# Kernel tuning notes

Measured on AMD Instinct MI355X. Metric: run time of the kernel, lower is better.

## Reference

```python
import jax, jax.numpy as jnp
import numpy as np

B, S, D, H = 2, 2048, 2048, 16
HD = D // H          # 128
HALF = HD // 2       # 64
EPS = 1e-6


def setup_inputs() -> dict:
    key = jax.random.key(0)
    ks = jax.random.split(key, 10)
    x = jax.random.normal(ks[0], (B, S, D), jnp.float32)
    # RoPE frequencies: standard theta=10000, per (position, half head dim)
    inv_freq = 1.0 / (10000.0 ** (np.arange(HALF, dtype=np.float64) / HALF))
    ang = np.outer(np.arange(S, dtype=np.float64), inv_freq)  # (S, HALF)
    freqs_cos = jnp.asarray(np.cos(ang), jnp.float32)[:, None, :]  # (S,1,HALF)
    freqs_sin = jnp.asarray(np.sin(ang), jnp.float32)[:, None, :]
    sc = 0.02
    qw = jax.random.normal(ks[1], (D, D), jnp.float32) * sc
    kw = jax.random.normal(ks[2], (D, D), jnp.float32) * sc
    vw = jax.random.normal(ks[3], (D, D), jnp.float32) * sc
    ow = jax.random.normal(ks[4], (D, D), jnp.float32) * sc
    qb = jax.random.normal(ks[5], (D,), jnp.float32) * sc
    kb = jax.random.normal(ks[6], (D,), jnp.float32) * sc
    vb = jax.random.normal(ks[7], (D,), jnp.float32) * sc
    ob = jax.random.normal(ks[8], (D,), jnp.float32) * sc
    qnorm_w = jnp.ones((D,), jnp.float32)
    knorm_w = jnp.ones((D,), jnp.float32)
    return {"x": x, "freqs_cos": freqs_cos, "freqs_sin": freqs_sin,
            "qw": qw, "qb": qb, "kw": kw, "kb": kb, "vw": vw, "vb": vb,
            "ow": ow, "ob": ob, "qnorm_w": qnorm_w, "knorm_w": knorm_w}


def _rmsnorm(h, w):
    # norm in fp32 over full last dim (dim, not per-head), as in the source
    hf = h.astype(jnp.float32)
    inv = jax.lax.rsqrt(jnp.mean(hf * hf, axis=-1, keepdims=True) + EPS)
    return (hf * inv).astype(h.dtype) * w


def _rope(h, cos, sin):
    # h: (B,S,D) -> complex rotation on interleaved pairs per head
    b, s, _ = h.shape
    hp = h.reshape(b, s, H, HALF, 2)
    x1, x2 = hp[..., 0], hp[..., 1]
    c = cos[None]   # (1,S,1,HALF) broadcasts over batch & heads
    sn = sin[None]
    o1 = x1 * c - x2 * sn
    o2 = x1 * sn + x2 * c
    return jnp.stack([o1, o2], axis=-1).reshape(b, s, H * HD)


def reference(x, freqs_cos, freqs_sin, qw, qb, kw, kb, vw, vb, ow, ob, qnorm_w, knorm_w):
    q = _rope(_rmsnorm(x @ qw.T + qb, qnorm_w), freqs_cos, freqs_sin)
    k = _rope(_rmsnorm(x @ kw.T + kb, knorm_w), freqs_cos, freqs_sin)
    v = x @ vw.T + vb
    b, s, _ = x.shape
    qh = q.reshape(b, s, H, HD)
    kh = k.reshape(b, s, H, HD)
    vh = v.reshape(b, s, H, HD)
    scale = 1.0 / jnp.sqrt(jnp.float32(HD))
    att = jnp.einsum('bqhd,bkhd->bhqk', qh, kh) * scale
    p = jax.nn.softmax(att, axis=-1)
    o = jnp.einsum('bhqk,bkhd->bqhd', p, vh).reshape(b, s, D)
    return o @ ow.T + ob
```

## Files before the change

### kernel.cpp

```cpp
#include <hip/hip_runtime.h>
#include <stdint.h>

#define B_SZ 2
#define S_LEN 2048
#define D_DIM 2048
#define NHEAD 16
#define HD 128
#define HALF 64
#define MROWS (B_SZ * S_LEN)

typedef __attribute__((ext_vector_type(8))) __bf16 bf16x8;
typedef __attribute__((ext_vector_type(8))) unsigned short u16x8;
typedef __attribute__((ext_vector_type(4))) float f32x4;
typedef __attribute__((ext_vector_type(16))) float f32x16;
typedef __attribute__((ext_vector_type(4))) unsigned int u32x4;

__device__ inline unsigned short f2bf(float x) {
  union { float f; uint32_t u; } c; c.f = x;
  uint32_t r = (c.u + 0x7fffu + ((c.u >> 16) & 1u)) >> 16;
  return (unsigned short)r;
}

__device__ inline float bf2f(unsigned short b) {
  union { uint32_t u; float f; } c; c.u = (uint32_t)b << 16;
  return c.f;
}

__device__ inline void gll16(const void* g, void* l) {
  __builtin_amdgcn_global_load_lds(
      (const __attribute__((address_space(1))) void*)g,
      (__attribute__((address_space(3))) void*)l,
      16, 0, 0);
}

__global__ void cast_all(const float* __restrict__ x,
                         const float* __restrict__ qw, const float* __restrict__ kw,
                         const float* __restrict__ vw, const float* __restrict__ ow,
                         unsigned short* __restrict__ xb,
                         unsigned short* __restrict__ qwb, unsigned short* __restrict__ kwb,
                         unsigned short* __restrict__ vwb, unsigned short* __restrict__ owb) {
  const int n_x = (MROWS * D_DIM) / 4;
  const int n_w = (D_DIM * D_DIM) / 4;
  const int total = n_x + 4 * n_w;
  int i = blockIdx.x * blockDim.x + threadIdx.x;
  int stride = gridDim.x * blockDim.x;
  for (; i < total; i += stride) {
    const float* src; unsigned short* dst; int off;
    if (i < n_x) { src = x; dst = xb; off = i; }
    else {
      int j = i - n_x;
      int seg = j >> 20;
      off = j & (n_w - 1);
      src = seg == 0 ? qw : seg == 1 ? kw : seg == 2 ? vw : ow;
      dst = seg == 0 ? qwb : seg == 1 ? kwb : seg == 2 ? vwb : owb;
    }
    float4 v = reinterpret_cast<const float4*>(src)[off];
    ushort4 o;
    o.x = f2bf(v.x); o.y = f2bf(v.y); o.z = f2bf(v.z); o.w = f2bf(v.w);
    reinterpret_cast<ushort4*>(dst)[off] = o;
  }
}

template <int MODE>
__global__ __launch_bounds__(256) void gemm_bt(
    const unsigned short* __restrict__ A, const unsigned short* __restrict__ Bt,
    const float* __restrict__ bias, void* __restrict__ Cv,
    int M, int N, int K) {
  __shared__ __align__(16) unsigned short As[128 * 32];
  __shared__ __align__(16) unsigned short Bs[128 * 32];
  const int tid = threadIdx.x;
  const int lane = tid & 63;
  const int wave = tid >> 6;
  const int nbn = N >> 7;
  const int chunk = gridDim.x >> 3;
  const int lin = (blockIdx.x & 7) * chunk + (blockIdx.x >> 3);
  const int bm = lin / nbn, bn = lin - bm * nbn;
  const int wr = wave >> 1, wc = wave & 1;
  const int lm = lane & 15, lg = lane >> 4;

  f32x4 acc[4][4] = {};

  for (int k0 = 0; k0 < K; k0 += 32) {
    __syncthreads();
#pragma unroll
    for (int j = 0; j < 2; ++j) {
      int ob = wave * 2048 + j * 1024;
      int o = ob + lane * 16;
      int row = o >> 6;
      int col = (o & 63) >> 1;
      const unsigned short* ga = A + (size_t)(bm * 128 + row) * K + k0 + col;
      gll16(ga, (char*)As + ob);
      const unsigned short* gb = Bt + (size_t)(bn * 128 + row) * K + k0 + col;
      gll16(gb, (char*)Bs + ob);
    }
    __syncthreads();

    bf16x8 af[4], bfr[4];
#pragma unroll
    for (int mi = 0; mi < 4; ++mi)
      af[mi] = *reinterpret_cast<const bf16x8*>(
          &As[(wr * 64 + mi * 16 + lm) * 32 + lg * 8]);
#pragma unroll
    for (int ni = 0; ni < 4; ++ni)
      bfr[ni] = *reinterpret_cast<const bf16x8*>(
          &Bs[(wc * 64 + ni * 16 + lm) * 32 + lg * 8]);
#pragma unroll
    for (int mi = 0; mi < 4; ++mi)
#pragma unroll
      for (int ni = 0; ni < 4; ++ni)
        acc[mi][ni] = __builtin_amdgcn_mfma_f32_16x16x32_bf16(
            af[mi], bfr[ni], acc[mi][ni], 0, 0, 0);
  }

#pragma unroll
  for (int ni = 0; ni < 4; ++ni) {
    int col = bn * 128 + wc * 64 + ni * 16 + lm;
    float bv = bias[col];
    if constexpr (MODE == 2) {
      int h = col >> 7, d = col & (HD - 1);
#pragma unroll
      for (int mi = 0; mi < 4; ++mi) {
        int row0 = bm * 128 + wr * 64 + mi * 16 + lg * 4;
        int b = row0 >> 11, s0 = row0 & (S_LEN - 1);
        ushort4 o;
        o.x = f2bf(acc[mi][ni][0] + bv);
        o.y = f2bf(acc[mi][ni][1] + bv);
        o.z = f2bf(acc[mi][ni][2] + bv);
        o.w = f2bf(acc[mi][ni][3] + bv);
        unsigned short* vt = (unsigned short*)Cv;
        size_t oi = ((((size_t)(b * NHEAD + h) * (S_LEN / 64) + (s0 >> 6)) * HD + d) << 6)
                    + (s0 & 63);
        *reinterpret_cast<ushort4*>(vt + oi) = o;
      }
    } else {
#pragma unroll
      for (int mi = 0; mi < 4; ++mi) {
#pragma unroll
        for (int r = 0; r < 4; ++r) {
          int row = bm * 128 + wr * 64 + mi * 16 + lg * 4 + r;
          float v = acc[mi][ni][r] + bv;
          if constexpr (MODE == 1)
            ((unsigned short*)Cv)[(size_t)row * N + col] = f2bf(v);
          else
            ((float*)Cv)[(size_t)row * N + col] = v;
        }
      }
    }
  }
}

template <int BLOCKED>
__global__ __launch_bounds__(256) void norm_rope(
    const unsigned short* __restrict__ h, const float* __restrict__ w,
    const float* __restrict__ cosb, const float* __restrict__ sinb,
    unsigned short* __restrict__ out, float outscale) {
  const int row = blockIdx.x;
  const int pos = row & (S_LEN - 1);
  const unsigned short* hr = h + (size_t)row * D_DIM;
  const int t = threadIdx.x;
  const int d = t * 8;

  u16x8 hv = *reinterpret_cast<const u16x8*>(hr + d);
  float a[8];
#pragma unroll
  for (int i = 0; i < 8; ++i) a[i] = bf2f(hv[i]);
  float ss = 0.f;
#pragma unroll
  for (int i = 0; i < 8; ++i) ss += a[i] * a[i];
#pragma unroll
  for (int off = 32; off > 0; off >>= 1) ss += __shfl_down(ss, off);
  __shared__ float red[4];
  if ((t & 63) == 0) red[t >> 6] = ss;
  __syncthreads();
  float tot = red[0] + red[1] + red[2] + red[3];
  float inv = rsqrtf(tot * (1.0f / D_DIM) + 1e-6f) * outscale;

  const int p = (d & (HD - 1)) >> 1;
  const float* cp = cosb + pos * HALF + p;
  const float* sp = sinb + pos * HALF + p;
  const float* wp = w + d;

  float c0 = cp[0], c1 = cp[1], c2 = cp[2], c3 = cp[3];
  float s0 = sp[0], s1 = sp[1], s2 = sp[2], s3 = sp[3];
#pragma unroll
  for (int i = 0; i < 8; ++i) a[i] = a[i] * inv * wp[i];
  u16x8 o;
  o[0] = f2bf(a[0] * c0 - a[1] * s0);
  o[1] = f2bf(a[0] * s0 + a[1] * c0);
  o[2] = f2bf(a[2] * c1 - a[3] * s1);
  o[3] = f2bf(a[2] * s1 + a[3] * c1);
  o[4] = f2bf(a[4] * c2 - a[5] * s2);
  o[5] = f2bf(a[4] * s2 + a[5] * c2);
  o[6] = f2bf(a[6] * c3 - a[7] * s3);
  o[7] = f2bf(a[6] * s3 + a[7] * c3);
  if constexpr (BLOCKED) {
    int hh = t >> 4;
    int dd = d & (HD - 1);
    size_t oi = (((size_t)((row >> 11) * NHEAD + hh) * S_LEN) + pos) * HD + dd;
    *reinterpret_cast<u16x8*>(out + oi) = o;
  } else {
    *reinterpret_cast<u16x8*>(out + (size_t)row * D_DIM + d) = o;
  }
}

__global__ __launch_bounds__(512) void attn_kernel(
    const unsigned short* __restrict__ Q, const unsigned short* __restrict__ Kh,
    const unsigned short* __restrict__ Vt, unsigned short* __restrict__ O) {
  const int idx = blockIdx.x;
  const int swz = (idx & 7) * 32 + (idx >> 3);
  const int qb = swz & 7;
  const int h = (swz >> 3) & 15;
  const int b = swz >> 7;

  const int tid = threadIdx.x;
  const int lane = tid & 63;
  const int wave = tid >> 6;
  const int l31 = lane & 31;
  const int hh = lane >> 5;

  const size_t qbase = (size_t)b * S_LEN * D_DIM + (size_t)h * HD;
  const size_t hbase = (size_t)(b * NHEAD + h) * S_LEN * HD;
  const int q0w = qb * 256 + wave * 32;

  __shared__ __align__(16) unsigned short Ks[2 * 64 * 128];
  __shared__ __align__(16) unsigned short Vs[128 * 64];

  bf16x8 qf[8];
#pragma unroll
  for (int ds_ = 0; ds_ < 8; ++ds_)
    qf[ds_] = *reinterpret_cast<const bf16x8*>(
        Q + qbase + (size_t)(q0w + l31) * D_DIM + ds_ * 16 + hh * 8);

  f32x16 oacc[4] = {};
  float mrow = -1e30f, lrow = 0.f;

  const int pbase = wave * 1024 + (lane << 4);

  auto stageK = [&](int buf, int tix) {
    const unsigned short* ksrc = Kh + hbase + (size_t)tix * (64 * HD);
#pragma unroll
    for (int j = 0; j < 2; ++j) {
      int p = pbase + j * 8192;
      int kr = p >> 8;
      int kc = ((p >> 4) & 15) ^ ((kr & 7) ^ ((kr >> 3) & 7));
      gll16(ksrc + kr * 128 + kc * 8, (char*)Ks + buf * 16384 + p);
    }
  };
  auto stageV = [&](int tix) {
    const unsigned short* vsrc = Vt + hbase + (size_t)tix * (64 * HD);
#pragma unroll
    for (int j = 0; j < 2; ++j) {
      int p = pbase + j * 8192;
      int vr = p >> 7;
      int vc = ((p >> 4) & 7) ^ (((vr & 7) ^ ((vr >> 3) & 7)) & 7);
      gll16(vsrc + vr * 64 + vc * 8, (char*)Vs + p);
    }
  };

  stageK(0, 0);

  const int NT = S_LEN / 64;
  for (int t = 0; t < NT; ++t) {
    const int cur = t & 1;
    stageV(t);
    stageK(cur ^ 1, (t + 1 < NT) ? t + 1 : t);
    asm volatile("s_waitcnt vmcnt(4)" ::: "memory");
    __builtin_amdgcn_sched_barrier(0);
    __builtin_amdgcn_s_barrier();
    __builtin_amdgcn_sched_barrier(0);

    const char* kbp = (const char*)Ks + cur * 16384;
    const int fk0 = (l31 & 7) ^ ((l31 >> 3) & 7);
    const int fk1 = (l31 & 7) ^ (((l31 + 32) >> 3) & 7);
    f32x16 pA = {}, pB = {};
    __builtin_amdgcn_s_setprio(1);
#pragma unroll
    for (int ds_ = 0; ds_ < 8; ++ds_) {
      bf16x8 k0 = *reinterpret_cast<const bf16x8*>(
          kbp + l31 * 256 + (((ds_ * 2 + hh) ^ fk0) << 4));
      bf16x8 k1 = *reinterpret_cast<const bf16x8*>(
          kbp + (32 + l31) * 256 + (((ds_ * 2 + hh) ^ fk1) << 4));
      pA = __builtin_amdgcn_mfma_f32_32x32x16_bf16(k0, qf[ds_], pA, 0, 0, 0);
      pB = __builtin_amdgcn_mfma_f32_32x32x16_bf16(k1, qf[ds_], pB, 0, 0, 0);
    }
    __builtin_amdgcn_s_setprio(0);

    float m8[8];
#pragma unroll
    for (int r = 0; r < 8; ++r)
      m8[r] = fmaxf(fmaxf(pA[r], pA[r + 8]), fmaxf(pB[r], pB[r + 8]));
#pragma unroll
    for (int r = 0; r < 4; ++r) m8[r] = fmaxf(m8[r], m8[r + 4]);
    float mx = fmaxf(fmaxf(m8[0], m8[1]), fmaxf(m8[2], m8[3]));
    mx = fmaxf(mx, __shfl_xor(mx, 32));
    if (__any(mx > mrow + 8.0f)) {
      float nm = fmaxf(mrow, mx);
      float alpha = exp2f(mrow - nm);
      mrow = nm;
      lrow *= alpha;
#pragma unroll
      for (int r = 0; r < 16; ++r) {
        int qr = (r & 3) + 8 * (r >> 2) + 4 * hh;
        float av = __shfl(alpha, qr);
        oacc[0][r] *= av; oacc[1][r] *= av; oacc[2][r] *= av; oacc[3][r] *= av;
      }
    }
#pragma unroll
    for (int r = 0; r < 16; ++r) pA[r] = exp2f(pA[r] - mrow);
#pragma unroll
    for (int r = 0; r < 16; ++r) pB[r] = exp2f(pB[r] - mrow);
    float s8[8];
#pragma unroll
    for (int r = 0; r < 8; ++r)
      s8[r] = (pA[r] + pA[r + 8]) + (pB[r] + pB[r + 8]);
#pragma unroll
    for (int r = 0; r < 4; ++r) s8[r] += s8[r + 4];
    lrow += (s8[0] + s8[1]) + (s8[2] + s8[3]);

    uint32_t w[16];
#pragma unroll
    for (int gg = 0; gg < 4; ++gg) {
      uint32_t lo, hi;
      float a0 = pA[4 * gg], a1 = pA[4 * gg + 1], a2 = pA[4 * gg + 2], a3 = pA[4 * gg + 3];
      asm("v_cvt_pk_bf16_f32 %0, %1, %2" : "=v"(lo) : "v"(a0), "v"(a1));
      asm("v_cvt_pk_bf16_f32 %0, %1, %2" : "=v"(hi) : "v"(a2), "v"(a3));
      w[gg * 2] = lo; w[gg * 2 + 1] = hi;
    }
#pragma unroll
    for (int gg = 0; gg < 4; ++gg) {
      uint32_t lo, hi;
      float a0 = pB[4 * gg], a1 = pB[4 * gg + 1], a2 = pB[4 * gg + 2], a3 = pB[4 * gg + 3];
      asm("v_cvt_pk_bf16_f32 %0, %1, %2" : "=v"(lo) : "v"(a0), "v"(a1));
      asm("v_cvt_pk_bf16_f32 %0, %1, %2" : "=v"(hi) : "v"(a2), "v"(a3));
      w[8 + gg * 2] = lo; w[8 + gg * 2 + 1] = hi;
    }
    bf16x8 pa[4];
#pragma unroll
    for (int s = 0; s < 4; ++s) {
      int wb = (s >> 1) * 8 + (s & 1) * 4;
      uint32_t le = w[wb], he = w[wb + 1], lo_ = w[wb + 2], ho = w[wb + 3];
      asm("v_permlane32_swap_b32 %0, %1" : "+v"(le), "+v"(lo_));
      asm("v_permlane32_swap_b32 %0, %1" : "+v"(he), "+v"(ho));
      u32x4 fr = {le, he, lo_, ho};
      pa[s] = __builtin_bit_cast(bf16x8, fr);
    }

    asm volatile("s_waitcnt vmcnt(2)" ::: "memory");
    __builtin_amdgcn_sched_barrier(0);
    __builtin_amdgcn_s_barrier();
    __builtin_amdgcn_sched_barrier(0);

    const char* vbp = (const char*)Vs;
    __builtin_amdgcn_s_setprio(1);
#pragma unroll
    for (int db = 0; db < 4; ++db) {
      int d = db * 32 + l31;
      int fv = (d & 7) ^ ((d >> 3) & 7);
#pragma unroll
      for (int ks = 0; ks < 4; ++ks) {
        bf16x8 vv = *reinterpret_cast<const bf16x8*>(
            vbp + d * 128 + (((ks * 2 + hh) ^ fv) << 4));
        oacc[db] = __builtin_amdgcn_mfma_f32_32x32x16_bf16(pa[ks], vv, oacc[db], 0, 0, 0);
      }
    }
    __builtin_amdgcn_s_setprio(0);

    __builtin_amdgcn_sched_barrier(0);
    __builtin_amdgcn_s_barrier();
    __builtin_amdgcn_sched_barrier(0);
  }

  lrow += __shfl_xor(lrow, 32);
  float inv_[16];
#pragma unroll
  for (int r = 0; r < 16; ++r) {
    int qr = (r & 3) + 8 * (r >> 2) + 4 * hh;
    inv_[r] = 1.0f / __shfl(lrow, qr);
  }
#pragma unroll
  for (int db = 0; db < 4; ++db) {
#pragma unroll
    for (int r = 0; r < 16; ++r) {
      int qr = (r & 3) + 8 * (r >> 2) + 4 * hh;
      O[qbase + (size_t)(q0w + qr) * D_DIM + db * 32 + l31] =
          f2bf(oacc[db][r] * inv_[r]);
    }
  }
}

extern "C" void kernel_launch(void* const* d_in, const int* in_sizes, int n_in,
                              void* d_out, int out_size, void* d_ws, size_t ws_size,
                              hipStream_t stream) {
  const float* x   = (const float*)d_in[0];
  const float* fc  = (const float*)d_in[1];
  const float* fs  = (const float*)d_in[2];
  const float* qw  = (const float*)d_in[3];
  const float* qb  = (const float*)d_in[4];
  const float* kw  = (const float*)d_in[5];
  const float* kb  = (const float*)d_in[6];
  const float* vw  = (const float*)d_in[7];
  const float* vb  = (const float*)d_in[8];
  const float* ow  = (const float*)d_in[9];
  const float* ob  = (const float*)d_in[10];
  const float* qnw = (const float*)d_in[11];
  const float* knw = (const float*)d_in[12];
  float* out = (float*)d_out;

  const size_t MSD = (size_t)MROWS * D_DIM;
  const size_t WSZ = (size_t)D_DIM * D_DIM;
  char* ws = (char*)d_ws;
  unsigned short* xb   = (unsigned short*)ws; ws += MSD * 2;
  unsigned short* qwb  = (unsigned short*)ws; ws += WSZ * 2;
  unsigned short* kwb  = (unsigned short*)ws; ws += WSZ * 2;
  unsigned short* vwb  = (unsigned short*)ws; ws += WSZ * 2;
  unsigned short* owb  = (unsigned short*)ws; ws += WSZ * 2;
  unsigned short* qpre = (unsigned short*)ws; ws += MSD * 2;
  unsigned short* qb16 = (unsigned short*)ws; ws += MSD * 2;
  unsigned short* kb16 = (unsigned short*)ws; ws += MSD * 2;
  unsigned short* vt16 = (unsigned short*)ws; ws += MSD * 2;
  unsigned short* ob16 = (unsigned short*)ws; ws += MSD * 2;

  cast_all<<<2048, 256, 0, stream>>>(x, qw, kw, vw, ow, xb, qwb, kwb, vwb, owb);

  dim3 ggrid((D_DIM / 128) * (MROWS / 128));
  gemm_bt<2><<<ggrid, 256, 0, stream>>>(xb, vwb, vb, vt16, MROWS, D_DIM, D_DIM);
  gemm_bt<1><<<ggrid, 256, 0, stream>>>(xb, qwb, qb, qpre, MROWS, D_DIM, D_DIM);
  const float qscale = 0.08838834764831845f * 1.4426950408889634f;
  norm_rope<0><<<MROWS, 256, 0, stream>>>(qpre, qnw, fc, fs, qb16, qscale);
  gemm_bt<1><<<ggrid, 256, 0, stream>>>(xb, kwb, kb, qpre, MROWS, D_DIM, D_DIM);
  norm_rope<1><<<MROWS, 256, 0, stream>>>(qpre, knw, fc, fs, kb16, 1.0f);

  attn_kernel<<<dim3(S_LEN / 256 * NHEAD * B_SZ), 512, 0, stream>>>(qb16, kb16, vt16, ob16);

  gemm_bt<0><<<ggrid, 256, 0, stream>>>(ob16, owb, ob, out, MROWS, D_DIM, D_DIM);
}
```

Baseline: 339.6 us.

## Fuse QKV projections into one triple-buffered 128x256 GEMM with swizzled LDS

Replaces the 128x128 single-buffered GEMM with a 128x256 tile, 512-thread kernel that stages K=64 slices into a three-slot LDS ring with XOR-swizzled rows and overlaps global loads with MFMA work. Q, K and V projections become one GEMM over the concatenated weights (qw, kw, vw laid out contiguously in the workspace) with a concatenated bias, routing output columns to separate Q/K/V buffers. This removes two launches, rereads of x, and global-to-LDS latency stalls. It relies on the three weight buffers being adjacent in memory and uses much more LDS per block, which lowers occupancy.

Result: slower. 348.6 us (+2.6%).

```diff
diff --git a/kernel.cpp b/kernel.cpp
--- a/kernel.cpp
+++ b/kernel.cpp
@@ -62,88 +62,127 @@
 }
 
 template <int MODE>
-__global__ __launch_bounds__(256) void gemm_bt(
+__global__ __launch_bounds__(512) void gemm256(
     const unsigned short* __restrict__ A, const unsigned short* __restrict__ Bt,
-    const float* __restrict__ bias, void* __restrict__ Cv,
+    const float* __restrict__ bias, void* __restrict__ C0,
+    unsigned short* __restrict__ C1, unsigned short* __restrict__ C2,
     int M, int N, int K) {
-  __shared__ __align__(16) unsigned short As[128 * 32];
-  __shared__ __align__(16) unsigned short Bs[128 * 32];
+  __shared__ __align__(16) unsigned short As[3 * 128 * 64];
+  __shared__ __align__(16) unsigned short Bs[3 * 256 * 64];
   const int tid = threadIdx.x;
   const int lane = tid & 63;
   const int wave = tid >> 6;
-  const int nbn = N >> 7;
+  const int lm = lane & 15, lg = lane >> 4;
+  const int nbn = N >> 8;
   const int chunk = gridDim.x >> 3;
   const int lin = (blockIdx.x & 7) * chunk + (blockIdx.x >> 3);
   const int bm = lin / nbn, bn = lin - bm * nbn;
-  const int wr = wave >> 1, wc = wave & 1;
-  const int lm = lane & 15, lg = lane >> 4;
+  const int mwave = (wave >> 2) * 64;
+  const int nwave = (wave & 3) * 64;
 
   f32x4 acc[4][4] = {};
 
-  for (int k0 = 0; k0 < K; k0 += 32) {
-    __syncthreads();
-#pragma unroll
-    for (int j = 0; j < 2; ++j) {
-      int ob = wave * 2048 + j * 1024;
-      int o = ob + lane * 16;
-      int row = o >> 6;
-      int col = (o & 63) >> 1;
-      const unsigned short* ga = A + (size_t)(bm * 128 + row) * K + k0 + col;
-      gll16(ga, (char*)As + ob);
-      const unsigned short* gb = Bt + (size_t)(bn * 128 + row) * K + k0 + col;
-      gll16(gb, (char*)Bs + ob);
-    }
-    __syncthreads();
-
-    bf16x8 af[4], bfr[4];
-#pragma unroll
-    for (int mi = 0; mi < 4; ++mi)
-      af[mi] = *reinterpret_cast<const bf16x8*>(
-          &As[(wr * 64 + mi * 16 + lm) * 32 + lg * 8]);
-#pragma unroll
-    for (int ni = 0; ni < 4; ++ni)
-      bfr[ni] = *reinterpret_cast<const bf16x8*>(
-          &Bs[(wc * 64 + ni * 16 + lm) * 32 + lg * 8]);
-#pragma unroll
-    for (int mi = 0; mi < 4; ++mi)
-#pragma unroll
-      for (int ni = 0; ni < 4; ++ni)
-        acc[mi][ni] = __builtin_amdgcn_mfma_f32_16x16x32_bf16(
-            af[mi], bfr[ni], acc[mi][ni], 0, 0, 0);
+  auto stage = [&](int slot, int kt) {
+    const int k0 = kt * 64;
+#pragma unroll
+    for (int r = 0; r < 2; ++r) {
+      int p = r * 8192 + tid * 16;
+      int row = p >> 7, ch = (p >> 4) & 7;
+      gll16(A + (size_t)(bm * 128 + row) * K + k0 + ((ch ^ (row & 7)) << 3),
+            (char*)As + slot * 16384 + p);
+    }
+#pragma unroll
+    for (int r = 0; r < 4; ++r) {
+      int p = r * 8192 + tid * 16;
+      int row = p >> 7, ch = (p >> 4) & 7;
+      gll16(Bt + (size_t)(bn * 256 + row) * K + k0 + ((ch ^ (row & 7)) << 3),
+            (char*)Bs + slot * 32768 + p);
+    }
+  };
+
+  const int NT = K >> 6;
+  stage(0, 0);
+  stage(1, 1 < NT ? 1 : 0);
+
+  int rd = 0, st = 2;
+  for (int t = 0; t < NT; ++t) {
+    stage(st, (t + 2 < NT) ? t + 2 : NT - 1);
+    asm volatile("s_waitcnt vmcnt(6)" ::: "memory");
+    __builtin_amdgcn_sched_barrier(0);
+    __builtin_amdgcn_s_barrier();
+    __builtin_amdgcn_sched_barrier(0);
+
+    const char* abp = (const char*)As + rd * 16384;
+    const char* bbp = (const char*)Bs + rd * 32768;
+#pragma unroll
+    for (int kk = 0; kk < 2; ++kk) {
+      bf16x8 af[4], bf[4];
+#pragma unroll
+      for (int mi = 0; mi < 4; ++mi) {
+        int row = mwave + mi * 16 + lm;
+        af[mi] = *reinterpret_cast<const bf16x8*>(
+            abp + row * 128 + ((((kk << 2) + lg) ^ (row & 7)) << 4));
+      }
+#pragma unroll
+      for (int ni = 0; ni < 4; ++ni) {
+        int row = nwave + ni * 16 + lm;
+        bf[ni] = *reinterpret_cast<const bf16x8*>(
+            bbp + row * 128 + ((((kk << 2) + lg) ^ (row & 7)) << 4));
+      }
+      __builtin_amdgcn_s_barrier();
+      __builtin_amdgcn_sched_barrier(0);
+      __builtin_amdgcn_s_setprio(1);
+#pragma unroll
+      for (int mi = 0; mi < 4; ++mi)
+#pragma unroll
+        for (int ni = 0; ni < 4; ++ni)
+          acc[mi][ni] = __builtin_amdgcn_mfma_f32_16x16x32_bf16(
+              af[mi], bf[ni], acc[mi][ni], 0, 0, 0);
+      __builtin_amdgcn_s_setprio(0);
+      __builtin_amdgcn_sched_barrier(0);
+      __builtin_amdgcn_s_barrier();
+      __builtin_amdgcn_sched_barrier(0);
+    }
+    rd = (rd == 2) ? 0 : rd + 1;
+    st = (st == 2) ? 0 : st + 1;
   }
 
 #pragma unroll
   for (int ni = 0; ni < 4; ++ni) {
-    int col = bn * 128 + wc * 64 + ni * 16 + lm;
+    int col = bn * 256 + nwave + ni * 16 + lm;
     float bv = bias[col];
-    if constexpr (MODE == 2) {
-      int h = col >> 7, d = col & (HD - 1);
+    if constexpr (MODE == 3) {
+      int seg = col >> 11;
+      int c2 = col & (D_DIM - 1);
 #pragma unroll
       for (int mi = 0; mi < 4; ++mi) {
-        int row0 = bm * 128 + wr * 64 + mi * 16 + lg * 4;
-        int b = row0 >> 11, s0 = row0 & (S_LEN - 1);
-        ushort4 o;
-        o.x = f2bf(acc[mi][ni][0] + bv);
-        o.y = f2bf(acc[mi][ni][1] + bv);
-        o.z = f2bf(acc[mi][ni][2] + bv);
-        o.w = f2bf(acc[mi][ni][3] + bv);
-        unsigned short* vt = (unsigned short*)Cv;
-        size_t oi = ((((size_t)(b * NHEAD + h) * (S_LEN / 64) + (s0 >> 6)) * HD + d) << 6)
-                    + (s0 & 63);
-        *reinterpret_cast<ushort4*>(vt + oi) = o;
+        int row0 = bm * 128 + mwave + mi * 16 + lg * 4;
+        if (seg == 2) {
+          int b = row0 >> 11, s0 = row0 & (S_LEN - 1);
+          int h = c2 >> 7, d = c2 & (HD - 1);
+          ushort4 o;
+          o.x = f2bf(acc[mi][ni][0] + bv);
+          o.y = f2bf(acc[mi][ni][1] + bv);
+          o.z = f2bf(acc[mi][ni][2] + bv);
+          o.w = f2bf(acc[mi][ni][3] + bv);
+          size_t oi = ((((size_t)(b * NHEAD + h) * (S_LEN / 64) + (s0 >> 6)) * HD + d) << 6)
+                      + (s0 & 63);
+          *reinterpret_cast<ushort4*>(C2 + oi) = o;
+        } else {
+          unsigned short* dst = (seg == 0) ? (unsigned short*)C0 : C1;
+#pragma unroll
+          for (int r = 0; r < 4; ++r)
+            dst[(size_t)(row0 + r) * D_DIM + c2] = f2bf(acc[mi][ni][r] + bv);
+        }
       }
     } else {
+      float* out = (float*)C0;
 #pragma unroll
       for (int mi = 0; mi < 4; ++mi) {
-#pragma unroll
-        for (int r = 0; r < 4; ++r) {
-          int row = bm * 128 + wr * 64 + mi * 16 + lg * 4 + r;
-          float v = acc[mi][ni][r] + bv;
-          if constexpr (MODE == 1)
-            ((unsigned short*)Cv)[(size_t)row * N + col] = f2bf(v);
-          else
-            ((float*)Cv)[(size_t)row * N + col] = v;
-        }
+        int row0 = bm * 128 + mwave + mi * 16 + lg * 4;
+#pragma unroll
+        for (int r = 0; r < 4; ++r)
+          out[(size_t)(row0 + r) * N + col] = acc[mi][ni][r] + bv;
       }
     }
   }
@@ -414,23 +453,28 @@
   unsigned short* kwb  = (unsigned short*)ws; ws += WSZ * 2;
   unsigned short* vwb  = (unsigned short*)ws; ws += WSZ * 2;
   unsigned short* owb  = (unsigned short*)ws; ws += WSZ * 2;
+  float*          cbias = (float*)ws;         ws += 3 * D_DIM * 4;
   unsigned short* qpre = (unsigned short*)ws; ws += MSD * 2;
+  unsigned short* kpre = (unsigned short*)ws; ws += MSD * 2;
   unsigned short* qb16 = (unsigned short*)ws; ws += MSD * 2;
   unsigned short* kb16 = (unsigned short*)ws; ws += MSD * 2;
   unsigned short* vt16 = (unsigned short*)ws; ws += MSD * 2;
   unsigned short* ob16 = (unsigned short*)ws; ws += MSD * 2;
 
   cast_all<<<2048, 256, 0, stream>>>(x, qw, kw, vw, ow, xb, qwb, kwb, vwb, owb);
-
-  dim3 ggrid((D_DIM / 128) * (MROWS / 128));
-  gemm_bt<2><<<ggrid, 256, 0, stream>>>(xb, vwb, vb, vt16, MROWS, D_DIM, D_DIM);
-  gemm_bt<1><<<ggrid, 256, 0, stream>>>(xb, qwb, qb, qpre, MROWS, D_DIM, D_DIM);
+  hipMemcpyAsync(cbias,              qb, D_DIM * sizeof(float), hipMemcpyDeviceToDevice, stream);
+  hipMemcpyAsync(cbias + D_DIM,      kb, D_DIM * sizeof(float), hipMemcpyDeviceToDevice, stream);
+  hipMemcpyAsync(cbias + 2 * D_DIM,  vb, D_DIM * sizeof(float), hipMemcpyDeviceToDevice, stream);
+
+  gemm256<3><<<dim3((MROWS / 128) * (3 * D_DIM / 256)), 512, 0, stream>>>(
+      xb, qwb, cbias, qpre, kpre, vt16, MROWS, 3 * D_DIM, D_DIM);
+
   const float qscale = 0.08838834764831845f * 1.4426950408889634f;
   norm_rope<0><<<MROWS, 256, 0, stream>>>(qpre, qnw, fc, fs, qb16, qscale);
-  gemm_bt<1><<<ggrid, 256, 0, stream>>>(xb, kwb, kb, qpre, MROWS, D_DIM, D_DIM);
-  norm_rope<1><<<MROWS, 256, 0, stream>>>(qpre, knw, fc, fs, kb16, 1.0f);
+  norm_rope<1><<<MROWS, 256, 0, stream>>>(kpre, knw, fc, fs, kb16, 1.0f);
 
   attn_kernel<<<dim3(S_LEN / 256 * NHEAD * B_SZ), 512, 0, stream>>>(qb16, kb16, vt16, ob16);
 
-  gemm_bt<0><<<ggrid, 256, 0, stream>>>(ob16, owb, ob, out, MROWS, D_DIM, D_DIM);
-}
+  gemm256<0><<<dim3((MROWS / 128) * (D_DIM / 256)), 512, 0, stream>>>(
+      ob16, owb, ob, out, nullptr, nullptr, MROWS, D_DIM, D_DIM);
+}
```
